# Performance work log

Measured on AMD Instinct MI355X. Metric: run time of the kernel, lower is better.

Reference implementation:

```python
import jax, jax.numpy as jnp
import numpy as np

N, F = 8000, 256
NEG_SLOPE = 0.2


def setup_inputs() -> dict:
    key = jax.random.key(0)
    k1, k2, k3, k4, k5, k6, k7 = jax.random.split(key, 7)
    node_embeddings = jax.random.normal(k1, (N, F), dtype=jnp.float32)
    adj_matrix = jax.random.randint(k2, (N, N), 0, 2, dtype=jnp.int32)
    # Learned params: W (Linear F->F with bias), a (Linear 2F->1 with bias).
    # a's weight [1, 2F] is split into a_src (first F, applied to H_i) and
    # a_dst (last F, applied to H_j) -- mathematically identical to the
    # concat-then-linear formulation, without the N*N*2F intermediate.
    s = 1.0 / np.sqrt(F)
    W_w = jax.random.uniform(k3, (F, F), dtype=jnp.float32, minval=-s, maxval=s)
    W_b = jax.random.uniform(k4, (F,), dtype=jnp.float32, minval=-s, maxval=s)
    s2 = 1.0 / np.sqrt(2 * F)
    a_src = jax.random.uniform(k5, (F,), dtype=jnp.float32, minval=-s2, maxval=s2)
    a_dst = jax.random.uniform(k6, (F,), dtype=jnp.float32, minval=-s2, maxval=s2)
    a_b = jax.random.uniform(k7, (), dtype=jnp.float32, minval=-s2, maxval=s2)
    return {
        "node_embeddings": node_embeddings,
        "adj_matrix": adj_matrix,
        "W_w": W_w,
        "W_b": W_b,
        "a_src": a_src,
        "a_dst": a_dst,
        "a_b": a_b,
    }


def reference(node_embeddings, adj_matrix, W_w, W_b, a_src, a_dst, a_b):
    # H = W(x)
    H = node_embeddings @ W_w.T + W_b                      # [N, F]
    # e_ij = a([H_i ; H_j]) = H_i . a_src + H_j . a_dst + b
    e = (H @ a_src)[:, None] + (H @ a_dst)[None, :] + a_b  # [N, N]
    # mask BEFORE leakyrelu (as in the original), then leakyrelu, then softmax
    e = jnp.where(adj_matrix == 0, -jnp.inf, e)
    e = jnp.where(e >= 0, e, NEG_SLOPE * e)                # leakyrelu(-inf) = -inf
    attn = jax.nn.softmax(e, axis=1)                       # [N, N]
    return attn @ H                                        # [N, F]
```

## Files before the change

### kernel.cpp

```cpp
#include <hip/hip_runtime.h>

#define NN 8000
#define FD 256
#define NEG_SLOPE 0.2f
#define BM 32
#define KT 64

typedef __bf16 bf16;
typedef __bf16 bf16x8 __attribute__((ext_vector_type(8)));
typedef __bf16 bf16x4 __attribute__((ext_vector_type(4)));
typedef float f32x4 __attribute__((ext_vector_type(4)));

__global__ __launch_bounds__(256) void k_linear(const float* __restrict__ X,
                                                const float* __restrict__ W,
                                                const float* __restrict__ b,
                                                bf16* __restrict__ Ht) {
    __shared__ float Xs[16][260];
    const int t = threadIdx.x;
    const int i0 = blockIdx.x * 16;
    #pragma unroll
    for (int r = 0; r < 16; ++r)
        Xs[r][t] = X[(size_t)(i0 + r) * FD + t];
    __syncthreads();
    const int f = t;
    float acc[16];
    const float bf_ = b[f];
    #pragma unroll
    for (int ii = 0; ii < 16; ++ii) acc[ii] = bf_;
    for (int k4 = 0; k4 < FD / 4; ++k4) {
        const float4 w4 = *(const float4*)&W[(size_t)f * FD + k4 * 4];
        #pragma unroll
        for (int ii = 0; ii < 16; ++ii) {
            const float4 x4 = *(const float4*)&Xs[ii][k4 * 4];
            acc[ii] += x4.x * w4.x + x4.y * w4.y + x4.z * w4.z + x4.w * w4.w;
        }
    }
    bf16x8 v0, v1;
    #pragma unroll
    for (int ii = 0; ii < 8; ++ii) { v0[ii] = (bf16)acc[ii]; v1[ii] = (bf16)acc[ii + 8]; }
    *(bf16x8*)&Ht[(size_t)f * NN + i0]     = v0;
    *(bf16x8*)&Ht[(size_t)f * NN + i0 + 8] = v1;
}

__global__ __launch_bounds__(256) void k_attn_vec(const bf16* __restrict__ Ht,
                                                  const float* __restrict__ a_src,
                                                  const float* __restrict__ a_dst,
                                                  const float* __restrict__ a_b,
                                                  float* __restrict__ hs,
                                                  float* __restrict__ hd) {
    __shared__ float psh[4][64], pdh[4][64];
    const int t = threadIdx.x;
    const int li = t & 63;
    const int q = t >> 6;
    const int i = blockIdx.x * 64 + li;
    float ps = 0.f, pd = 0.f;
    #pragma unroll 8
    for (int fi = 0; fi < 64; ++fi) {
        const int f = q * 64 + fi;
        const float h = (float)Ht[(size_t)f * NN + i];
        ps += h * a_src[f];
        pd += h * a_dst[f];
    }
    psh[q][li] = ps; pdh[q][li] = pd;
    __syncthreads();
    if (q == 0) {
        ps = psh[0][li] + psh[1][li] + psh[2][li] + psh[3][li];
        pd = pdh[0][li] + pdh[1][li] + pdh[2][li] + pdh[3][li];
        hs[i] = ps + a_b[0];
        hd[i] = pd;
    }
}

__global__ __launch_bounds__(512, 4) void k_gat(const bf16* __restrict__ Ht,
                                                const int* __restrict__ adj,
                                                const float* __restrict__ hs,
                                                const float* __restrict__ hd,
                                                float* __restrict__ out,
                                                float* __restrict__ lg) {
    __shared__ __attribute__((aligned(16))) bf16 Bt[2][FD * KT];
    __shared__ __attribute__((aligned(16))) bf16 Wt[2][BM * KT];

    const int t  = threadIdx.x;
    const int l  = t & 63;
    const int wv = t >> 6;
    const int ib = blockIdx.x >> 1;
    const int jb = blockIdx.x & 1;
    const int i0 = ib * BM;
    const int jq0 = jb * 4032;
    const int NS = 63 - jb;

    const int r  = t >> 4;
    const int jm = (t & 15) * 4;
    const float hsv = hs[i0 + r];
    const int woff = r * KT + (((jm >> 3) ^ (r & 7)) << 3) + (((jm >> 2) & 1) << 2);
    const int* adjp  = adj + (size_t)(i0 + r) * NN + jq0 + jm;
    const float* hdp = hd + jq0 + jm;

    const int al = l & 15, asl = l >> 4;
    const int cswz = al & 7;
    const int colb = wv * 32 + al;

    auto stage = [&](int s_, int bufi) {
        #pragma unroll
        for (int q = 0; q < 4; ++q) {
            const int idx = q * 512 + t;
            const int col = idx >> 3;
            const int sslot = (idx & 7) ^ (col & 7);
            const bf16* src = Ht + (size_t)col * NN + jq0 + s_ * KT + sslot * 8;
            bf16* dst = &Bt[bufi][(size_t)(q * 512 + wv * 64) * 8];
            __builtin_amdgcn_global_load_lds(
                (const __attribute__((address_space(1))) void*)src,
                (__attribute__((address_space(3))) void*)dst, 16, 0, 0);
        }
    };

    stage(0, 0);
    int4   adjc = *(const int4*)adjp;
    float4 hdc  = *(const float4*)hdp;

    f32x4 acc00 = {0.f, 0.f, 0.f, 0.f}, acc01 = acc00, acc10 = acc00, acc11 = acc00;
    f32x4 acc20 = acc00, acc21 = acc00, acc30 = acc00, acc31 = acc00;
    float lsum = 0.f;

    #pragma unroll 1
    for (int s = 0; s < NS; ++s) {
        const int cur = s & 1;
        int4 adjn; float4 hdn;
        if (s + 1 < NS) {
            stage(s + 1, cur ^ 1);
            adjn = *(const int4*)(adjp + (size_t)(s + 1) * KT);
            hdn  = *(const float4*)(hdp + (size_t)(s + 1) * KT);
            asm volatile("s_waitcnt vmcnt(6)" ::: "memory");
        } else {
            asm volatile("s_waitcnt vmcnt(0)" ::: "memory");
        }

        {
            float e, w0, w1, w2, w3;
            e = hsv + hdc.x; e = e >= 0.f ? e : NEG_SLOPE * e; w0 = adjc.x ? __expf(e) : 0.f;
            e = hsv + hdc.y; e = e >= 0.f ? e : NEG_SLOPE * e; w1 = adjc.y ? __expf(e) : 0.f;
            e = hsv + hdc.z; e = e >= 0.f ? e : NEG_SLOPE * e; w2 = adjc.z ? __expf(e) : 0.f;
            e = hsv + hdc.w; e = e >= 0.f ? e : NEG_SLOPE * e; w3 = adjc.w ? __expf(e) : 0.f;
            lsum += (w0 + w1) + (w2 + w3);
            bf16x4 wp; wp[0] = (bf16)w0; wp[1] = (bf16)w1; wp[2] = (bf16)w2; wp[3] = (bf16)w3;
            *(bf16x4*)&Wt[cur][woff] = wp;
        }
        asm volatile("s_waitcnt lgkmcnt(0)" ::: "memory");
        __builtin_amdgcn_s_barrier();

        {
            const bf16* wb = Wt[cur];
            const bf16* bb = Bt[cur];
            const bf16x8 a00 = *(const bf16x8*)&wb[(al)      * KT + (((0 + asl) ^ cswz) << 3)];
            const bf16x8 a01 = *(const bf16x8*)&wb[(al)      * KT + (((4 + asl) ^ cswz) << 3)];
            const bf16x8 a10 = *(const bf16x8*)&wb[(al + 16) * KT + (((0 + asl) ^ cswz) << 3)];
            const bf16x8 a11 = *(const bf16x8*)&wb[(al + 16) * KT + (((4 + asl) ^ cswz) << 3)];
            const bf16x8 b00 = *(const bf16x8*)&bb[(colb)      * KT + (((0 + asl) ^ cswz) << 3)];
            const bf16x8 b01 = *(const bf16x8*)&bb[(colb)      * KT + (((4 + asl) ^ cswz) << 3)];
            const bf16x8 b10 = *(const bf16x8*)&bb[(colb + 16) * KT + (((0 + asl) ^ cswz) << 3)];
            const bf16x8 b11 = *(const bf16x8*)&bb[(colb + 16) * KT + (((4 + asl) ^ cswz) << 3)];
            acc00 = __builtin_amdgcn_mfma_f32_16x16x32_bf16(a00, b00, acc00, 0, 0, 0);
            acc00 = __builtin_amdgcn_mfma_f32_16x16x32_bf16(a01, b01, acc00, 0, 0, 0);
            acc01 = __builtin_amdgcn_mfma_f32_16x16x32_bf16(a00, b10, acc01, 0, 0, 0);
            acc01 = __builtin_amdgcn_mfma_f32_16x16x32_bf16(a01, b11, acc01, 0, 0, 0);
            acc10 = __builtin_amdgcn_mfma_f32_16x16x32_bf16(a10, b00, acc10, 0, 0, 0);
            acc10 = __builtin_amdgcn_mfma_f32_16x16x32_bf16(a11, b01, acc10, 0, 0, 0);
            acc11 = __builtin_amdgcn_mfma_f32_16x16x32_bf16(a10, b10, acc11, 0, 0, 0);
            acc11 = __builtin_amdgcn_mfma_f32_16x16x32_bf16(a11, b11, acc11, 0, 0, 0);
        }
        asm volatile("s_waitcnt lgkmcnt(0)" ::: "memory");
        __builtin_amdgcn_s_barrier();

        adjc = adjn; hdc = hdn;
    }

    lsum += __shfl_xor(lsum, 1);
    lsum += __shfl_xor(lsum, 2);
    lsum += __shfl_xor(lsum, 4);
    lsum += __shfl_xor(lsum, 8);
    if ((t & 15) == 0) atomicAdd(&lg[i0 + r], lsum);

    #pragma unroll
    for (int g = 0; g < 4; ++g) {
        const int rr = asl * 4 + g;
        atomicAdd(&out[(size_t)(i0 + rr) * FD + wv * 32 + al],           acc00[g]);
        atomicAdd(&out[(size_t)(i0 + rr) * FD + wv * 32 + 16 + al],      acc01[g]);
        atomicAdd(&out[(size_t)(i0 + 16 + rr) * FD + wv * 32 + al],      acc10[g]);
        atomicAdd(&out[(size_t)(i0 + 16 + rr) * FD + wv * 32 + 16 + al], acc11[g]);
    }
    (void)acc20; (void)acc21; (void)acc30; (void)acc31;
}

__global__ __launch_bounds__(256) void k_norm(float* __restrict__ out,
                                              const float* __restrict__ lg) {
    const int i = blockIdx.x;
    const float rinv = 1.0f / lg[i];
    out[(size_t)i * FD + threadIdx.x] *= rinv;
}

extern "C" void kernel_launch(void* const* d_in, const int* in_sizes, int n_in,
                              void* d_out, int out_size, void* d_ws, size_t ws_size,
                              hipStream_t stream) {
    const float* X     = (const float*)d_in[0];
    const int*   adj   = (const int*)d_in[1];
    const float* Ww    = (const float*)d_in[2];
    const float* Wb    = (const float*)d_in[3];
    const float* a_src = (const float*)d_in[4];
    const float* a_dst = (const float*)d_in[5];
    const float* a_b   = (const float*)d_in[6];
    float* out = (float*)d_out;

    bf16*  Ht = (bf16*)d_ws;
    float* hs = (float*)((char*)d_ws + (size_t)FD * NN * sizeof(bf16));
    float* hd = hs + NN;
    float* lg = hd + NN;

    hipMemsetAsync(out, 0, (size_t)NN * FD * sizeof(float), stream);
    hipMemsetAsync(lg, 0, NN * sizeof(float), stream);

    k_linear<<<NN / 16, 256, 0, stream>>>(X, Ww, Wb, Ht);
    k_attn_vec<<<NN / 64, 256, 0, stream>>>(Ht, a_src, a_dst, a_b, hs, hd);
    k_gat<<<(NN / BM) * 2, 512, 0, stream>>>(Ht, adj, hs, hd, out, lg);
    k_norm<<<NN, 256, 0, stream>>>(out, lg);
}
```

Measured before the change: 151.8 us.

## Retile GAT kernel to 64-row blocks with 4-way j-split and fold memsets

```diff
diff --git a/kernel.cpp b/kernel.cpp
--- a/kernel.cpp
+++ b/kernel.cpp
@@ -3,8 +3,10 @@
 #define NN 8000
 #define FD 256
 #define NEG_SLOPE 0.2f
-#define BM 32
-#define KT 64
+#define BM 64
+#define KT 32
+#define JS 4
+#define CHUNK 2016
 
 typedef __bf16 bf16;
 typedef __bf16 bf16x8 __attribute__((ext_vector_type(8)));
@@ -14,10 +16,20 @@
 __global__ __launch_bounds__(256) void k_linear(const float* __restrict__ X,
                                                 const float* __restrict__ W,
                                                 const float* __restrict__ b,
-                                                bf16* __restrict__ Ht) {
+                                                bf16* __restrict__ Ht,
+                                                float* __restrict__ out,
+                                                float* __restrict__ lg) {
     __shared__ float Xs[16][260];
     const int t = threadIdx.x;
     const int i0 = blockIdx.x * 16;
+    {
+        const int gt = blockIdx.x * 256 + t;
+        const float4 z4 = {0.f, 0.f, 0.f, 0.f};
+        float4* o4 = (float4*)out;
+        #pragma unroll
+        for (int k = 0; k < 4; ++k) o4[gt + k * 128000] = z4;
+        if (gt < NN) lg[gt] = 0.f;
+    }
     #pragma unroll
     for (int r = 0; r < 16; ++r)
         Xs[r][t] = X[(size_t)(i0 + r) * FD + t];
@@ -83,43 +95,46 @@
     const int t  = threadIdx.x;
     const int l  = t & 63;
     const int wv = t >> 6;
-    const int ib = blockIdx.x >> 1;
-    const int jb = blockIdx.x & 1;
+    const int ib = blockIdx.x >> 2;
+    const int jb = blockIdx.x & 3;
     const int i0 = ib * BM;
-    const int jq0 = jb * 4032;
-    const int NS = 63 - jb;
-
-    const int r  = t >> 4;
-    const int jm = (t & 15) * 4;
+    const int jq0 = jb * CHUNK;
+    const int NS = (jb < 3) ? 63 : 61;
+
+    const int r  = t >> 3;
+    const int jm = (t & 7) << 2;
     const float hsv = hs[i0 + r];
-    const int woff = r * KT + (((jm >> 3) ^ (r & 7)) << 3) + (((jm >> 2) & 1) << 2);
     const int* adjp  = adj + (size_t)(i0 + r) * NN + jq0 + jm;
     const float* hdp = hd + jq0 + jm;
+    const int woff = r * 64 + (((jm >> 3) ^ ((r >> 2) & 3)) << 4) + (((jm >> 2) & 1) << 3);
 
     const int al = l & 15, asl = l >> 4;
-    const int cswz = al & 7;
-    const int colb = wv * 32 + al;
+    const int eff = (asl ^ ((al >> 2) & 3)) << 4;
 
     auto stage = [&](int s_, int bufi) {
         #pragma unroll
-        for (int q = 0; q < 4; ++q) {
+        for (int q = 0; q < 2; ++q) {
             const int idx = q * 512 + t;
-            const int col = idx >> 3;
-            const int sslot = (idx & 7) ^ (col & 7);
-            const bf16* src = Ht + (size_t)col * NN + jq0 + s_ * KT + sslot * 8;
-            bf16* dst = &Bt[bufi][(size_t)(q * 512 + wv * 64) * 8];
+            const int col = idx >> 2;
+            const int kk = (idx & 3) ^ ((col >> 2) & 3);
+            const bf16* src = Ht + (size_t)col * NN + jq0 + s_ * KT + kk * 8;
+            bf16* dst = &Bt[bufi][(q * 512 + wv * 64) * 8];
             __builtin_amdgcn_global_load_lds(
                 (const __attribute__((address_space(1))) void*)src,
                 (__attribute__((address_space(3))) void*)dst, 16, 0, 0);
         }
     };
 
-    stage(0, 0);
     int4   adjc = *(const int4*)adjp;
     float4 hdc  = *(const float4*)hdp;
-
-    f32x4 acc00 = {0.f, 0.f, 0.f, 0.f}, acc01 = acc00, acc10 = acc00, acc11 = acc00;
-    f32x4 acc20 = acc00, acc21 = acc00, acc30 = acc00, acc31 = acc00;
+    stage(0, 0);
+
+    f32x4 acc[4][2];
+    #pragma unroll
+    for (int sr = 0; sr < 4; ++sr) {
+        acc[sr][0] = (f32x4){0.f, 0.f, 0.f, 0.f};
+        acc[sr][1] = (f32x4){0.f, 0.f, 0.f, 0.f};
+    }
     float lsum = 0.f;
 
     #pragma unroll 1
@@ -127,12 +142,9 @@
         const int cur = s & 1;
         int4 adjn; float4 hdn;
         if (s + 1 < NS) {
-            stage(s + 1, cur ^ 1);
             adjn = *(const int4*)(adjp + (size_t)(s + 1) * KT);
             hdn  = *(const float4*)(hdp + (size_t)(s + 1) * KT);
-            asm volatile("s_waitcnt vmcnt(6)" ::: "memory");
-        } else {
-            asm volatile("s_waitcnt vmcnt(0)" ::: "memory");
+            stage(s + 1, cur ^ 1);
         }
 
         {
@@ -143,30 +155,29 @@
             e = hsv + hdc.w; e = e >= 0.f ? e : NEG_SLOPE * e; w3 = adjc.w ? __expf(e) : 0.f;
             lsum += (w0 + w1) + (w2 + w3);
             bf16x4 wp; wp[0] = (bf16)w0; wp[1] = (bf16)w1; wp[2] = (bf16)w2; wp[3] = (bf16)w3;
-            *(bf16x4*)&Wt[cur][woff] = wp;
-        }
+            *(bf16x4*)((char*)&Wt[cur][0] + woff) = wp;
+        }
+
+        if (s + 1 < NS) asm volatile("s_waitcnt vmcnt(4)" ::: "memory");
+        else            asm volatile("s_waitcnt vmcnt(0)" ::: "memory");
         asm volatile("s_waitcnt lgkmcnt(0)" ::: "memory");
         __builtin_amdgcn_s_barrier();
 
         {
-            const bf16* wb = Wt[cur];
-            const bf16* bb = Bt[cur];
-            const bf16x8 a00 = *(const bf16x8*)&wb[(al)      * KT + (((0 + asl) ^ cswz) << 3)];
-            const bf16x8 a01 = *(const bf16x8*)&wb[(al)      * KT + (((4 + asl) ^ cswz) << 3)];
-            const bf16x8 a10 = *(const bf16x8*)&wb[(al + 16) * KT + (((0 + asl) ^ cswz) << 3)];
-            const bf16x8 a11 = *(const bf16x8*)&wb[(al + 16) * KT + (((4 + asl) ^ cswz) << 3)];
-            const bf16x8 b00 = *(const bf16x8*)&bb[(colb)      * KT + (((0 + asl) ^ cswz) << 3)];
-            const bf16x8 b01 = *(const bf16x8*)&bb[(colb)      * KT + (((4 + asl) ^ cswz) << 3)];
-            const bf16x8 b10 = *(const bf16x8*)&bb[(colb + 16) * KT + (((0 + asl) ^ cswz) << 3)];
-            const bf16x8 b11 = *(const bf16x8*)&bb[(colb + 16) * KT + (((4 + asl) ^ cswz) << 3)];
-            acc00 = __builtin_amdgcn_mfma_f32_16x16x32_bf16(a00, b00, acc00, 0, 0, 0);
-            acc00 = __builtin_amdgcn_mfma_f32_16x16x32_bf16(a01, b01, acc00, 0, 0, 0);
-            acc01 = __builtin_amdgcn_mfma_f32_16x16x32_bf16(a00, b10, acc01, 0, 0, 0);
-            acc01 = __builtin_amdgcn_mfma_f32_16x16x32_bf16(a01, b11, acc01, 0, 0, 0);
-            acc10 = __builtin_amdgcn_mfma_f32_16x16x32_bf16(a10, b00, acc10, 0, 0, 0);
-            acc10 = __builtin_amdgcn_mfma_f32_16x16x32_bf16(a11, b01, acc10, 0, 0, 0);
-            acc11 = __builtin_amdgcn_mfma_f32_16x16x32_bf16(a10, b10, acc11, 0, 0, 0);
-            acc11 = __builtin_amdgcn_mfma_f32_16x16x32_bf16(a11, b11, acc11, 0, 0, 0);
+            const char* wb = (const char*)&Wt[cur][0];
+            const char* bb = (const char*)&Bt[cur][0];
+            bf16x8 a[4], b[2];
+            #pragma unroll
+            for (int sr = 0; sr < 4; ++sr)
+                a[sr] = *(const bf16x8*)(wb + (sr * 16 + al) * 64 + eff);
+            #pragma unroll
+            for (int cf = 0; cf < 2; ++cf)
+                b[cf] = *(const bf16x8*)(bb + (wv * 32 + cf * 16 + al) * 64 + eff);
+            #pragma unroll
+            for (int sr = 0; sr < 4; ++sr) {
+                acc[sr][0] = __builtin_amdgcn_mfma_f32_16x16x32_bf16(a[sr], b[0], acc[sr][0], 0, 0, 0);
+                acc[sr][1] = __builtin_amdgcn_mfma_f32_16x16x32_bf16(a[sr], b[1], acc[sr][1], 0, 0, 0);
+            }
         }
         asm volatile("s_waitcnt lgkmcnt(0)" ::: "memory");
         __builtin_amdgcn_s_barrier();
@@ -177,18 +188,19 @@
     lsum += __shfl_xor(lsum, 1);
     lsum += __shfl_xor(lsum, 2);
     lsum += __shfl_xor(lsum, 4);
-    lsum += __shfl_xor(lsum, 8);
-    if ((t & 15) == 0) atomicAdd(&lg[i0 + r], lsum);
-
-    #pragma unroll
-    for (int g = 0; g < 4; ++g) {
-        const int rr = asl * 4 + g;
-        atomicAdd(&out[(size_t)(i0 + rr) * FD + wv * 32 + al],           acc00[g]);
-        atomicAdd(&out[(size_t)(i0 + rr) * FD + wv * 32 + 16 + al],      acc01[g]);
-        atomicAdd(&out[(size_t)(i0 + 16 + rr) * FD + wv * 32 + al],      acc10[g]);
-        atomicAdd(&out[(size_t)(i0 + 16 + rr) * FD + wv * 32 + 16 + al], acc11[g]);
-    }
-    (void)acc20; (void)acc21; (void)acc30; (void)acc31;
+    if ((t & 7) == 0) atomicAdd(&lg[i0 + r], lsum);
+
+    #pragma unroll
+    for (int sr = 0; sr < 4; ++sr) {
+        #pragma unroll
+        for (int cf = 0; cf < 2; ++cf) {
+            #pragma unroll
+            for (int g = 0; g < 4; ++g) {
+                atomicAdd(&out[(size_t)(i0 + sr * 16 + asl * 4 + g) * FD + wv * 32 + cf * 16 + al],
+                          acc[sr][cf][g]);
+            }
+        }
+    }
 }
 
 __global__ __launch_bounds__(256) void k_norm(float* __restrict__ out,
@@ -215,11 +227,8 @@
     float* hd = hs + NN;
     float* lg = hd + NN;
 
-    hipMemsetAsync(out, 0, (size_t)NN * FD * sizeof(float), stream);
-    hipMemsetAsync(lg, 0, NN * sizeof(float), stream);
-
-    k_linear<<<NN / 16, 256, 0, stream>>>(X, Ww, Wb, Ht);
+    k_linear<<<NN / 16, 256, 0, stream>>>(X, Ww, Wb, Ht, out, lg);
     k_attn_vec<<<NN / 64, 256, 0, stream>>>(Ht, a_src, a_dst, a_b, hs, hd);
-    k_gat<<<(NN / BM) * 2, 512, 0, stream>>>(Ht, adj, hs, hd, out, lg);
+    k_gat<<<(NN / BM) * JS, 512, 0, stream>>>(Ht, adj, hs, hd, out, lg);
     k_norm<<<NN, 256, 0, stream>>>(out, lg);
 }
```

After: 150.9 us. Within noise of the previous version (-0.6%).
